# Kernel optimization log

Hardware: AMD Instinct MI355X
Metric: run time of the kernel (lower is better)

## Reference

```python
import jax, jax.numpy as jnp
import numpy as np

DILATION = 64
KERNEL = 2

def setup_inputs() -> dict:
    key = jax.random.key(0)
    k1, k2 = jax.random.split(key)
    x = jax.random.normal(k1, (16, 64, 16384), dtype=jnp.float32)
    w = jax.random.normal(k2, (64, 64, KERNEL), dtype=jnp.float32) * 0.1
    return {"x": x, "w": w}

def _causal_dilated_conv(x, w):
    # left-pad by dilation*(kernel_size-1) for causality
    pad = DILATION * (KERNEL - 1)
    xp = jnp.pad(x, ((0, 0), (0, 0), (pad, 0)))
    return jax.lax.conv_general_dilated(
        xp, w,
        window_strides=(1,),
        padding='VALID',
        rhs_dilation=(DILATION,),
        dimension_numbers=('NCH', 'OIH', 'NCH'))

def reference(x, w):
    y = _causal_dilated_conv(x, w)          # [B, C_out, T]
    return jnp.tanh(y) * jax.nn.sigmoid(y)  # fused gate
```

## Files before the change

kernel.cpp:

```cpp
#include <hip/hip_runtime.h>


#define B_ 16
#define C_ 64
#define T_ 16384

typedef __attribute__((ext_vector_type(8))) short short8;
typedef __attribute__((ext_vector_type(4))) float f32x4;

union Frag { short8 s; unsigned u[4]; };

__device__ __forceinline__ unsigned bf16_rne(float f) {
    unsigned u = __float_as_uint(f);
    return (u + 0x7fffu + ((u >> 16) & 1u)) >> 16;
}

__device__ __forceinline__ unsigned pack_rne(float a, float b) {
    unsigned ua = __float_as_uint(a), ub = __float_as_uint(b);
    unsigned ra = ua + 0x7fffu + ((ua >> 16) & 1u);
    unsigned rb = ub + 0x7fffu + ((ub >> 16) & 1u);
    return (ra >> 16) | (rb & 0xffff0000u);
}

#define EPILOGUE(A, KK)                                                     \
    _Pragma("unroll")                                                       \
    for (int s = 0; s < 4; ++s) {                                           \
        float4 o4;                                                          \
        _Pragma("unroll")                                                   \
        for (int r = 0; r < 4; ++r) {                                       \
            float y = fmaxf((A)[s][r], -30.f);                              \
            float u = __expf(-y);                                           \
            ((float*)&o4)[r] = (1.f - u) *                                  \
                __builtin_amdgcn_rcpf(__builtin_fmaf(u, u, 1.f));           \
        }                                                                   \
        *(float4*)(ob + (KK) * 64 + 16 * s + 4 * q) = o4;                   \
    }

__global__ __launch_bounds__(256, 4) void conv_gate_pipe(
    const float* __restrict__ x,
    const float* __restrict__ w,
    float* __restrict__ out)
{
    __shared__ unsigned short xs[3 * 64 * 64];

    const int tid = threadIdx.x;
    const int bid = blockIdx.x;
    const int wg  = (bid & 7) * 128 + (bid >> 3);
    const int b   = wg >> 6;
    const int seg = wg & 63;
    const int t0  = seg << 8;
    const float* xb = x + (size_t)b * C_ * T_;

    float pv[4][8];
    #pragma unroll
    for (int it = 0; it < 4; ++it) {
        const int task = it * 256 + tid;
        const int rr   = task & 127;
        const int c8   = task >> 7;
        const int g    = t0 - 64 + rr;
        if (g >= 0) {
            const float* xp = xb + (size_t)(8 * c8) * T_ + g;
            #pragma unroll
            for (int i = 0; i < 8; ++i) pv[it][i] = xp[(size_t)i * T_];
        } else {
            #pragma unroll
            for (int i = 0; i < 8; ++i) pv[it][i] = 0.f;
        }
    }

    float vbuf[2][2][8];
    #pragma unroll
    for (int it = 0; it < 2; ++it) {
        const int task = it * 256 + tid;
        const int rr = task & 63, c8 = task >> 6;
        const float* xp = xb + (size_t)(8 * c8) * T_ + (t0 + 64 + rr);
        #pragma unroll
        for (int i = 0; i < 8; ++i) vbuf[0][it][i] = xp[(size_t)i * T_];
    }

    const int lane = tid & 63;
    const int wid  = tid >> 6;
    const int m    = lane & 15;
    const int q    = lane >> 4;
    const int co   = wid * 16 + m;

    Frag wh[2][2], wl[2][2];
    #pragma unroll
    for (int h = 0; h < 2; ++h) {
        const float* wp = w + co * 128 + h * 64 + q * 16;
        float f[16];
        #pragma unroll
        for (int v4 = 0; v4 < 4; ++v4) {
            float4 t4 = *(const float4*)(wp + 4 * v4);
            f[4*v4+0] = t4.x; f[4*v4+1] = t4.y; f[4*v4+2] = t4.z; f[4*v4+3] = t4.w;
        }
        #pragma unroll
        for (int p = 0; p < 2; ++p) {
            #pragma unroll
            for (int d = 0; d < 4; ++d) {
                float e0 = f[2*(2*d)   + p];
                float e1 = f[2*(2*d+1) + p];
                unsigned h0 = bf16_rne(e0), h1 = bf16_rne(e1);
                float r0 = e0 - __uint_as_float(h0 << 16);
                float r1 = e1 - __uint_as_float(h1 << 16);
                wh[p][h].u[d] = h0 | (h1 << 16);
                wl[p][h].u[d] = bf16_rne(r0) | (bf16_rne(r1) << 16);
            }
        }
    }

    #pragma unroll
    for (int it = 0; it < 4; ++it) {
        const int task = it * 256 + tid;
        const int rr   = task & 127;
        const int c8   = task >> 7;
        unsigned p0 = pack_rne(pv[it][0], pv[it][1]);
        unsigned p1 = pack_rne(pv[it][2], pv[it][3]);
        unsigned p2 = pack_rne(pv[it][4], pv[it][5]);
        unsigned p3 = pack_rne(pv[it][6], pv[it][7]);
        const int so = (rr >> 6) * 4096 + (rr & 63) * 64 + ((c8 ^ (rr & 7)) * 8);
        *(uint4*)(&xs[so]) = make_uint4(p0, p1, p2, p3);
    }

    const int n   = m;
    const int swb = n & 7;
    float* ob = out + ((size_t)b * C_ + wid * 16 + m) * T_ + t0;

    f32x4 acc2[2][4];

    __syncthreads();

    #pragma unroll
    for (int k = 0; k < 4; ++k) {
        if (k <= 1) {
            #pragma unroll
            for (int it = 0; it < 2; ++it) {
                const int task = it * 256 + tid;
                const int rr = task & 63, c8 = task >> 6;
                const float* xp = xb + (size_t)(8 * c8) * T_ + (t0 + 64 * (k + 2) + rr);
                #pragma unroll
                for (int i = 0; i < 8; ++i) vbuf[(k + 1) & 1][it][i] = xp[(size_t)i * T_];
            }
        }

        if (k >= 1) { EPILOGUE(acc2[(k & 1) ^ 1], k - 1); }

        if (k <= 2) {
            #pragma unroll
            for (int it = 0; it < 2; ++it) {
                const int task = it * 256 + tid;
                const int rr = task & 63, c8 = task >> 6;
                unsigned p0 = pack_rne(vbuf[k & 1][it][0], vbuf[k & 1][it][1]);
                unsigned p1 = pack_rne(vbuf[k & 1][it][2], vbuf[k & 1][it][3]);
                unsigned p2 = pack_rne(vbuf[k & 1][it][4], vbuf[k & 1][it][5]);
                unsigned p3 = pack_rne(vbuf[k & 1][it][6], vbuf[k & 1][it][7]);
                const int so = ((k + 2) % 3) * 4096 + rr * 64 + ((c8 ^ (rr & 7)) * 8);
                *(uint4*)(&xs[so]) = make_uint4(p0, p1, p2, p3);
            }
        }

        f32x4* acc = acc2[k & 1];
        #pragma unroll
        for (int s = 0; s < 4; ++s) acc[s] = (f32x4){0.f, 0.f, 0.f, 0.f};
        #pragma unroll
        for (int u = 0; u < 8; ++u) {
            const int wnd   = k + (u >> 2);
            const int rbase = (wnd % 3) * 4096 + (16 * (u & 3) + n) * 64;
            Frag f0, f1;
            f0.s = *(const short8*)(&xs[rbase + ((q ^ swb) * 8)]);
            f1.s = *(const short8*)(&xs[rbase + (((4 + q) ^ swb) * 8)]);
            if (u < 4) {
                acc[u] = __builtin_amdgcn_mfma_f32_16x16x32_bf16(f0.s, wh[0][0].s, acc[u], 0, 0, 0);
                acc[u] = __builtin_amdgcn_mfma_f32_16x16x32_bf16(f0.s, wl[0][0].s, acc[u], 0, 0, 0);
                acc[u] = __builtin_amdgcn_mfma_f32_16x16x32_bf16(f1.s, wh[0][1].s, acc[u], 0, 0, 0);
                acc[u] = __builtin_amdgcn_mfma_f32_16x16x32_bf16(f1.s, wl[0][1].s, acc[u], 0, 0, 0);
            } else {
                const int s2 = u - 4;
                acc[s2] = __builtin_amdgcn_mfma_f32_16x16x32_bf16(f0.s, wh[1][0].s, acc[s2], 0, 0, 0);
                acc[s2] = __builtin_amdgcn_mfma_f32_16x16x32_bf16(f0.s, wl[1][0].s, acc[s2], 0, 0, 0);
                acc[s2] = __builtin_amdgcn_mfma_f32_16x16x32_bf16(f1.s, wh[1][1].s, acc[s2], 0, 0, 0);
                acc[s2] = __builtin_amdgcn_mfma_f32_16x16x32_bf16(f1.s, wl[1][1].s, acc[s2], 0, 0, 0);
            }
        }

        if (k < 3) __syncthreads();
    }

    EPILOGUE(acc2[1], 3);
}

extern "C" void kernel_launch(void* const* d_in, const int* in_sizes, int n_in,
                              void* d_out, int out_size, void* d_ws, size_t ws_size,
                              hipStream_t stream) {
    const float* x = (const float*)d_in[0];
    const float* w = (const float*)d_in[1];
    float* out = (float*)d_out;
    conv_gate_pipe<<<dim3(1024), dim3(256), 0, stream>>>(x, w, out);
}
```

Measured before the change: 126.8 us.

## Load x tiles with float4 vector loads and defer LDS staging after MFMA

Replaces the scalar per-element global loads of x (8 channels per thread, one time index) with float4 loads covering 4 time steps across 4 channels per thread, then transposes in registers and writes uint2 packed bf16 into the swizzled LDS layout. The staging write of the next window is moved after the MFMA loop, so the global load latency overlaps the epilogue and the matrix math. This cuts the number of load instructions and widens each memory transaction. In exchange it uses narrower LDS writes and may introduce more bank conflicts, and it keeps more registers live across the MFMA loop.

```diff
diff --git a/kernel.cpp b/kernel.cpp
--- a/kernel.cpp
+++ b/kernel.cpp
@@ -36,7 +36,20 @@
         *(float4*)(ob + (KK) * 64 + 16 * s + 4 * q) = o4;                   \
     }
 
-__global__ __launch_bounds__(256, 4) void conv_gate_pipe(
+#define STAGE_WRITE(F, BANK)                                                \
+    _Pragma("unroll")                                                       \
+    for (int e = 0; e < 4; ++e) {                                           \
+        const int rr = 4 * tq + e;                                          \
+        const int so = (BANK) * 4096 + rr * 64 +                            \
+                       (((c4 >> 1) ^ (rr & 7)) * 8) + ((c4 & 1) * 4);       \
+        unsigned u0 = pack_rne(((const float*)&(F)[0])[e],                  \
+                               ((const float*)&(F)[1])[e]);                 \
+        unsigned u1 = pack_rne(((const float*)&(F)[2])[e],                  \
+                               ((const float*)&(F)[3])[e]);                 \
+        *(uint2*)(&xs[so]) = make_uint2(u0, u1);                            \
+    }
+
+__global__ __launch_bounds__(256, 4) void conv_gate_wide(
     const float* __restrict__ x,
     const float* __restrict__ w,
     float* __restrict__ out)
@@ -51,32 +64,22 @@
     const int t0  = seg << 8;
     const float* xb = x + (size_t)b * C_ * T_;
 
-    float pv[4][8];
+    const int c4 = tid >> 4;
+    const int tq = tid & 15;
+    const float* xgb = xb + (size_t)(4 * c4) * T_ + 4 * tq;
+
+    float4 fa[4], fb[4];
+    if (seg > 0) {
+        #pragma unroll
+        for (int i = 0; i < 4; ++i)
+            fa[i] = *(const float4*)(xgb + (size_t)i * T_ + (t0 - 64));
+    } else {
+        #pragma unroll
+        for (int i = 0; i < 4; ++i) fa[i] = make_float4(0.f, 0.f, 0.f, 0.f);
+    }
     #pragma unroll
-    for (int it = 0; it < 4; ++it) {
-        const int task = it * 256 + tid;
-        const int rr   = task & 127;
-        const int c8   = task >> 7;
-        const int g    = t0 - 64 + rr;
-        if (g >= 0) {
-            const float* xp = xb + (size_t)(8 * c8) * T_ + g;
-            #pragma unroll
-            for (int i = 0; i < 8; ++i) pv[it][i] = xp[(size_t)i * T_];
-        } else {
-            #pragma unroll
-            for (int i = 0; i < 8; ++i) pv[it][i] = 0.f;
-        }
-    }
-
-    float vbuf[2][2][8];
-    #pragma unroll
-    for (int it = 0; it < 2; ++it) {
-        const int task = it * 256 + tid;
-        const int rr = task & 63, c8 = task >> 6;
-        const float* xp = xb + (size_t)(8 * c8) * T_ + (t0 + 64 + rr);
-        #pragma unroll
-        for (int i = 0; i < 8; ++i) vbuf[0][it][i] = xp[(size_t)i * T_];
-    }
+    for (int i = 0; i < 4; ++i)
+        fb[i] = *(const float4*)(xgb + (size_t)i * T_ + t0);
 
     const int lane = tid & 63;
     const int wid  = tid >> 6;
@@ -109,18 +112,8 @@
         }
     }
 
-    #pragma unroll
-    for (int it = 0; it < 4; ++it) {
-        const int task = it * 256 + tid;
-        const int rr   = task & 127;
-        const int c8   = task >> 7;
-        unsigned p0 = pack_rne(pv[it][0], pv[it][1]);
-        unsigned p1 = pack_rne(pv[it][2], pv[it][3]);
-        unsigned p2 = pack_rne(pv[it][4], pv[it][5]);
-        unsigned p3 = pack_rne(pv[it][6], pv[it][7]);
-        const int so = (rr >> 6) * 4096 + (rr & 63) * 64 + ((c8 ^ (rr & 7)) * 8);
-        *(uint4*)(&xs[so]) = make_uint4(p0, p1, p2, p3);
-    }
+    STAGE_WRITE(fa, 0)
+    STAGE_WRITE(fb, 1)
 
     const int n   = m;
     const int swb = n & 7;
@@ -132,32 +125,14 @@
 
     #pragma unroll
     for (int k = 0; k < 4; ++k) {
-        if (k <= 1) {
+        float4 fv[4];
+        if (k <= 2) {
             #pragma unroll
-            for (int it = 0; it < 2; ++it) {
-                const int task = it * 256 + tid;
-                const int rr = task & 63, c8 = task >> 6;
-                const float* xp = xb + (size_t)(8 * c8) * T_ + (t0 + 64 * (k + 2) + rr);
-                #pragma unroll
-                for (int i = 0; i < 8; ++i) vbuf[(k + 1) & 1][it][i] = xp[(size_t)i * T_];
-            }
+            for (int i = 0; i < 4; ++i)
+                fv[i] = *(const float4*)(xgb + (size_t)i * T_ + (t0 + 64 * (k + 1)));
         }
 
         if (k >= 1) { EPILOGUE(acc2[(k & 1) ^ 1], k - 1); }
-
-        if (k <= 2) {
-            #pragma unroll
-            for (int it = 0; it < 2; ++it) {
-                const int task = it * 256 + tid;
-                const int rr = task & 63, c8 = task >> 6;
-                unsigned p0 = pack_rne(vbuf[k & 1][it][0], vbuf[k & 1][it][1]);
-                unsigned p1 = pack_rne(vbuf[k & 1][it][2], vbuf[k & 1][it][3]);
-                unsigned p2 = pack_rne(vbuf[k & 1][it][4], vbuf[k & 1][it][5]);
-                unsigned p3 = pack_rne(vbuf[k & 1][it][6], vbuf[k & 1][it][7]);
-                const int so = ((k + 2) % 3) * 4096 + rr * 64 + ((c8 ^ (rr & 7)) * 8);
-                *(uint4*)(&xs[so]) = make_uint4(p0, p1, p2, p3);
-            }
-        }
 
         f32x4* acc = acc2[k & 1];
         #pragma unroll
@@ -183,6 +158,8 @@
             }
         }
 
+        if (k <= 2) { STAGE_WRITE(fv, (k + 2) % 3) }
+
         if (k < 3) __syncthreads();
     }
 
@@ -195,5 +172,5 @@
     const float* x = (const float*)d_in[0];
     const float* w = (const float*)d_in[1];
     float* out = (float*)d_out;
-    conv_gate_pipe<<<dim3(1024), dim3(256), 0, stream>>>(x, w, out);
+    conv_gate_wide<<<dim3(1024), dim3(256), 0, stream>>>(x, w, out);
 }
```

After: 123.8 us. 2.4% less time.
